# Optimization experiments

Hardware: AMD Instinct MI355X
Metric: run time of the kernel (lower is better)

## Reference

```python
import jax, jax.numpy as jnp
import numpy as np

K = 3          # kernel_size (local window)
PAD = 1        # padding = (K-1)//2 -> 'same' output size
GROUPS = 8
C_OUT = 64


def _unfold3d(x, k):
    """x: [B,C,Dp,Hp,Wp] -> [B,C,D,H,W,kd,kh,kw] sliding windows (stride 1)."""
    B, C, Dp, Hp, Wp = x.shape
    D, H, W = Dp - k + 1, Hp - k + 1, Wp - k + 1
    idx_d = jnp.arange(D)[:, None] + jnp.arange(k)[None, :]
    idx_h = jnp.arange(H)[:, None] + jnp.arange(k)[None, :]
    idx_w = jnp.arange(W)[:, None] + jnp.arange(k)[None, :]
    x = x[:, :, idx_d]              # [B,C,D,kd,Hp,Wp]
    x = x[:, :, :, :, idx_h]        # [B,C,D,kd,H,kh,Wp]
    x = x[:, :, :, :, :, :, idx_w]  # [B,C,D,kd,H,kh,W,kw]
    return jnp.transpose(x, (0, 1, 2, 4, 6, 3, 5, 7))


def setup_inputs() -> dict:
    key = jax.random.key(0)
    ks = jax.random.split(key, 7)
    B, Cin, D, H, W = 1, 64, 16, 64, 64
    c3 = C_OUT // 3                 # 21
    rest = C_OUT - 2 * c3           # 22
    fan_out_scale = np.sqrt(2.0 / C_OUT)  # kaiming_normal fan_out, relu
    x = jax.random.normal(ks[0], (B, Cin, D, H, W), dtype=jnp.float32)
    w_q = jax.random.normal(ks[1], (C_OUT, Cin), dtype=jnp.float32) * fan_out_scale
    w_k = jax.random.normal(ks[2], (C_OUT, Cin), dtype=jnp.float32) * fan_out_scale
    w_v = jax.random.normal(ks[3], (C_OUT, Cin), dtype=jnp.float32) * fan_out_scale
    rel_d = jax.random.normal(ks[4], (c3, 1, 1, 1, K, 1, 1), dtype=jnp.float32)
    rel_h = jax.random.normal(ks[5], (c3, 1, 1, 1, 1, K, 1), dtype=jnp.float32)
    rel_w = jax.random.normal(ks[6], (rest, 1, 1, 1, 1, 1, K), dtype=jnp.float32)
    return {"x": x, "w_q": w_q, "w_k": w_k, "w_v": w_v,
            "rel_d": rel_d, "rel_h": rel_h, "rel_w": rel_w}


def reference(x, w_q, w_k, w_v, rel_d, rel_h, rel_w):
    B, Cin, D, H, W = x.shape
    cg = C_OUT // GROUPS
    c3 = C_OUT // 3
    # 1x1x1 convs (bias=False): plain channel mixing. conv(pad(x)) == pad(conv(x)).
    q = jnp.einsum('oc,bcdhw->bodhw', w_q, x)
    k = jnp.einsum('oc,bcdhw->bodhw', w_k, x)
    v = jnp.einsum('oc,bcdhw->bodhw', w_v, x)
    pad = [(0, 0), (0, 0), (PAD, PAD), (PAD, PAD), (PAD, PAD)]
    k = jnp.pad(k, pad)
    v = jnp.pad(v, pad)
    k_win = _unfold3d(k, K)   # [B,Co,D,H,W,kd,kh,kw]
    v_win = _unfold3d(v, K)
    # split relative position bias across channel thirds
    k_win = jnp.concatenate([
        k_win[:, :c3] + rel_d,
        k_win[:, c3:2 * c3] + rel_h,
        k_win[:, 2 * c3:] + rel_w,
    ], axis=1)
    Kv = K * K * K
    k_win = k_win.reshape(B, GROUPS, cg, D, H, W, Kv)
    v_win = v_win.reshape(B, GROUPS, cg, D, H, W, Kv)
    qg = q.reshape(B, GROUPS, cg, D, H, W, 1)
    attn = jax.nn.softmax(qg * k_win, axis=-1)
    out = jnp.einsum('bncdhwk,bncdhwk->bncdhw', attn, v_win)
    return out.reshape(B, C_OUT, D, H, W)
```

## Files before the change

### kernel.cpp

```cpp
#include <hip/hip_runtime.h>

#define SP    65536
#define DD    16
#define HH    64
#define WW    64
#define CIN   64
#define COUT  64

#define XP    132
#define WP    68

#define LOG2E 1.44269504f


__global__ __launch_bounds__(256) void proj(const float* __restrict__ x,
                                            const float* __restrict__ wq,
                                            const float* __restrict__ wk,
                                            const float* __restrict__ wv,
                                            float* __restrict__ q,
                                            float* __restrict__ k,
                                            float* __restrict__ v) {
    __shared__ float xl[CIN][XP];
    __shared__ float wl[COUT][WP];

    const int t  = threadIdx.x;
    const int p0 = blockIdx.x * 128;
    const int m  = blockIdx.y;

    const float* __restrict__ wsel = (m == 0) ? wq : (m == 1) ? wk : wv;
    float* __restrict__       osel = (m == 0) ? q  : (m == 1) ? k  : v;

#pragma unroll
    for (int i = 0; i < 8; ++i) {
        const int f = t + 256 * i;
        const int c = f >> 5, j = f & 31;
        *(float4*)(&xl[c][j * 4]) = *(const float4*)(x + c * SP + p0 + j * 4);
    }
#pragma unroll
    for (int i = 0; i < 4; ++i) {
        const int f = t + 256 * i;
        const int o = f >> 4, j = f & 15;
        *(float4*)(&wl[o][j * 4]) = *(const float4*)(wsel + o * CIN + j * 4);
    }
    __syncthreads();

    const int og    = t >> 5;
    const int pg    = t & 31;
    const int obase = og * 8;
    const int pbase = pg * 4;

    float acc[8][4] = {};
#pragma unroll 2
    for (int c4 = 0; c4 < CIN / 4; ++c4) {
        float4 w4[8], x4[4];
#pragma unroll
        for (int i = 0; i < 8; ++i)
            w4[i] = *(const float4*)(&wl[obase + i][c4 * 4]);
#pragma unroll
        for (int cc = 0; cc < 4; ++cc)
            x4[cc] = *(const float4*)(&xl[c4 * 4 + cc][pbase]);
#pragma unroll
        for (int i = 0; i < 8; ++i) {
            const float* wf = (const float*)&w4[i];
#pragma unroll
            for (int cc = 0; cc < 4; ++cc) {
                const float* xf = (const float*)&x4[cc];
                const float wv_ = wf[cc];
                acc[i][0] = fmaf(wv_, xf[0], acc[i][0]);
                acc[i][1] = fmaf(wv_, xf[1], acc[i][1]);
                acc[i][2] = fmaf(wv_, xf[2], acc[i][2]);
                acc[i][3] = fmaf(wv_, xf[3], acc[i][3]);
            }
        }
    }

#pragma unroll
    for (int i = 0; i < 8; ++i)
        *(float4*)(osel + (obase + i) * SP + p0 + pbase) =
            make_float4(acc[i][0], acc[i][1], acc[i][2], acc[i][3]);
}

__device__ __forceinline__ float dpp_shr1(float x) {
    return __int_as_float(__builtin_amdgcn_mov_dpp(__float_as_int(x), 0x111, 0xf, 0xf, true));
}
__device__ __forceinline__ float dpp_shl1(float x) {
    return __int_as_float(__builtin_amdgcn_mov_dpp(__float_as_int(x), 0x101, 0xf, 0xf, true));
}

template<int AXIS>
__device__ __forceinline__ void attn_tile(const float* __restrict__ kt,
                                          const float* __restrict__ vt,
                                          const float (&ql)[2][4],
                                          float r0, float r1, float r2,
                                          int wg, int h, int dg,
                                          float (&s)[2][4], float (&a)[2][4]) {
#pragma unroll
    for (int nl = 0; nl < 4; ++nl) {
#pragma unroll
        for (int kh = 0; kh < 3; ++kh) {
            const int off = ((dg * 2 + nl) * 10 + h + kh) * 64 + wg * 4;
            const float4 km = *(const float4*)(kt + off);
            const float4 vm = *(const float4*)(vt + off);
            const float kl = dpp_shr1(km.w), kr = dpp_shl1(km.x);
            const float vl = dpp_shr1(vm.w), vr = dpp_shl1(vm.x);
            const float krow[6] = { kl, km.x, km.y, km.z, km.w, kr };
            const float vrow[6] = { vl, vm.x, vm.y, vm.z, vm.w, vr };

            const float rkh = (kh == 0) ? r0 : (kh == 1) ? r1 : r2;

#pragma unroll
            for (int di = 0; di < 2; ++di) {
                const int kd = nl - di;
                if (kd >= 0 && kd < 3) {
                    const float rdd = (kd == 0) ? r0 : (kd == 1) ? r1 : r2;
                    const float rr  = (AXIS == 0) ? rdd : (AXIS == 1) ? rkh : 0.f;
#pragma unroll
                    for (int wi = 0; wi < 4; ++wi) {
                        const float qv = ql[di][wi];
#pragma unroll
                        for (int kw = 0; kw < 3; ++kw) {
                            const float rc = (AXIS == 2)
                                           ? ((kw == 0) ? r0 : (kw == 1) ? r1 : r2)
                                           : rr;
                            const float e = __builtin_amdgcn_exp2f(qv * (krow[wi + kw] + rc));
                            s[di][wi] += e;
                            a[di][wi] = fmaf(e, vrow[wi + kw], a[di][wi]);
                        }
                    }
                }
            }
        }
    }
}

__global__ __launch_bounds__(256) void attn(const float* __restrict__ kbuf,
                                            const float* __restrict__ vbuf,
                                            const float* __restrict__ qbuf,
                                            const float* __restrict__ rel_d,
                                            const float* __restrict__ rel_h,
                                            const float* __restrict__ rel_w,
                                            float* __restrict__ out) {
    __shared__ float kt[60 * 64];
    __shared__ float vt[60 * 64];

    const int dt = blockIdx.x;
    const int ht = blockIdx.y;
    const int o  = blockIdx.z;

    const int d0 = dt * 4;
    const int h0 = ht * 8;
    const int t  = threadIdx.x;

    const float* __restrict__ kc = kbuf + o * SP;
    const float* __restrict__ vc = vbuf + o * SP;

#pragma unroll
    for (int i = 0; i < 8; ++i) {
        const int idx = t + 256 * i;
        if (idx < 1920) {
            const bool isv = idx >= 960;
            const int rem  = isv ? idx - 960 : idx;
            const int row  = rem >> 4;
            const int j    = rem & 15;
            const int nn   = row / 10;
            const int hp   = row - nn * 10;
            const int dpg  = d0 - 1 + nn;
            const int hpg  = h0 - 1 + hp;
            float4 val = make_float4(0.f, 0.f, 0.f, 0.f);
            if ((unsigned)dpg < (unsigned)DD && (unsigned)hpg < (unsigned)HH) {
                const float* src = (isv ? vc : kc) + (dpg * HH + hpg) * WW + j * 4;
                val = *(const float4*)src;
            }
            *(float4*)((isv ? vt : kt) + row * 64 + j * 4) = val;
        }
    }

    const int wg = t & 15;
    const int h  = (t >> 4) & 7;
    const int dg = t >> 7;

    float ql[2][4];
#pragma unroll
    for (int di = 0; di < 2; ++di) {
        const int dabs = d0 + dg * 2 + di;
        const float4 q4 = *(const float4*)(qbuf + o * SP + (dabs * HH + (h0 + h)) * WW + wg * 4);
        ql[di][0] = q4.x * LOG2E; ql[di][1] = q4.y * LOG2E;
        ql[di][2] = q4.z * LOG2E; ql[di][3] = q4.w * LOG2E;
    }

    __syncthreads();

    float s[2][4] = {};
    float a[2][4] = {};

    if (o < 21) {
        attn_tile<0>(kt, vt, ql, rel_d[o * 3 + 0], rel_d[o * 3 + 1], rel_d[o * 3 + 2],
                     wg, h, dg, s, a);
    } else if (o < 42) {
        const int b = o - 21;
        attn_tile<1>(kt, vt, ql, rel_h[b * 3 + 0], rel_h[b * 3 + 1], rel_h[b * 3 + 2],
                     wg, h, dg, s, a);
    } else {
        const int b = o - 42;
        attn_tile<2>(kt, vt, ql, rel_w[b * 3 + 0], rel_w[b * 3 + 1], rel_w[b * 3 + 2],
                     wg, h, dg, s, a);
    }

#pragma unroll
    for (int di = 0; di < 2; ++di) {
        const int dabs = d0 + dg * 2 + di;
        float4 ov;
        ov.x = a[di][0] * __builtin_amdgcn_rcpf(s[di][0]);
        ov.y = a[di][1] * __builtin_amdgcn_rcpf(s[di][1]);
        ov.z = a[di][2] * __builtin_amdgcn_rcpf(s[di][2]);
        ov.w = a[di][3] * __builtin_amdgcn_rcpf(s[di][3]);
        *(float4*)(out + o * SP + (dabs * HH + (h0 + h)) * WW + wg * 4) = ov;
    }
}

extern "C" void kernel_launch(void* const* d_in, const int* in_sizes, int n_in,
                              void* d_out, int out_size, void* d_ws, size_t ws_size,
                              hipStream_t stream) {
    const float* x     = (const float*)d_in[0];
    const float* w_q   = (const float*)d_in[1];
    const float* w_k   = (const float*)d_in[2];
    const float* w_v   = (const float*)d_in[3];
    const float* rel_d = (const float*)d_in[4];
    const float* rel_h = (const float*)d_in[5];
    const float* rel_w = (const float*)d_in[6];
    float* out = (float*)d_out;

    float* ws = (float*)d_ws;
    float* q  = ws;
    float* k  = ws + (size_t)COUT * SP;
    float* v  = ws + 2 * (size_t)COUT * SP;

    proj<<<dim3(SP / 128, 3), 256, 0, stream>>>(x, w_q, w_k, w_v, q, k, v);
    attn<<<dim3(4, 8, 64), 256, 0, stream>>>(k, v, q, rel_d, rel_h, rel_w, out);
}
```

Measured before the change: 125.7 us.

## Compute QKV projection with split-bf16 MFMA instead of FP32 FMAs

The 1x1x1 projection kernel now splits weights and inputs into hi/lo bf16 pairs in shared memory and uses 16x16x32 bf16 MFMA instructions (three products per tile: hi*hi, hi*lo, lo*hi) to approximate FP32 precision. This replaces the scalar FMA register-tiled GEMM and moves its arithmetic onto the matrix cores. In exchange it adds conversion work during staging, transposed scalar LDS stores that may bank-conflict, and uncoalesced scalar output stores. It also gives up a little accuracy relative to a true FP32 product.

```diff
diff --git a/kernel.cpp b/kernel.cpp
--- a/kernel.cpp
+++ b/kernel.cpp
@@ -7,11 +7,23 @@
 #define CIN   64
 #define COUT  64
 
-#define XP    132
-#define WP    68
-
 #define LOG2E 1.44269504f
 
+#define WPITCH 72
+#define XPITCH 72
+
+typedef short short8 __attribute__((ext_vector_type(8)));
+typedef float floatx4 __attribute__((ext_vector_type(4)));
+
+
+__device__ __forceinline__ float b2f(unsigned short u) {
+    return __uint_as_float(((unsigned)u) << 16);
+}
+__device__ __forceinline__ unsigned short f2b(float f) {
+    union { float f; unsigned u; } c; c.f = f;
+    unsigned r = c.u + 0x7fff + ((c.u >> 16) & 1);
+    return (unsigned short)(r >> 16);
+}
 
 __global__ __launch_bounds__(256) void proj(const float* __restrict__ x,
                                             const float* __restrict__ wq,
@@ -20,8 +32,10 @@
                                             float* __restrict__ q,
                                             float* __restrict__ k,
                                             float* __restrict__ v) {
-    __shared__ float xl[CIN][XP];
-    __shared__ float wl[COUT][WP];
+    __shared__ unsigned short whi[COUT * WPITCH];
+    __shared__ unsigned short wlo[COUT * WPITCH];
+    __shared__ unsigned short xhi[128 * XPITCH];
+    __shared__ unsigned short xlo[128 * XPITCH];
 
     const int t  = threadIdx.x;
     const int p0 = blockIdx.x * 128;
@@ -33,51 +47,78 @@
 #pragma unroll
     for (int i = 0; i < 8; ++i) {
         const int f = t + 256 * i;
-        const int c = f >> 5, j = f & 31;
-        *(float4*)(&xl[c][j * 4]) = *(const float4*)(x + c * SP + p0 + j * 4);
+        const int c = f >> 5;
+        const int j = f & 31;
+        const float4 val = *(const float4*)(x + c * SP + p0 + j * 4);
+        const float vf[4] = { val.x, val.y, val.z, val.w };
+#pragma unroll
+        for (int e = 0; e < 4; ++e) {
+            const int p = j * 4 + e;
+            const unsigned short h = f2b(vf[e]);
+            const float lof = vf[e] - b2f(h);
+            xhi[p * XPITCH + c] = h;
+            xlo[p * XPITCH + c] = f2b(lof);
+        }
     }
 #pragma unroll
     for (int i = 0; i < 4; ++i) {
-        const int f = t + 256 * i;
-        const int o = f >> 4, j = f & 15;
-        *(float4*)(&wl[o][j * 4]) = *(const float4*)(wsel + o * CIN + j * 4);
+        const int f  = t + 256 * i;
+        const int o  = f >> 4;
+        const int jc = f & 15;
+        const float4 val = *(const float4*)(wsel + o * CIN + jc * 4);
+        const float vf[4] = { val.x, val.y, val.z, val.w };
+        ushort4 h4, l4;
+        unsigned short* hp = (unsigned short*)&h4;
+        unsigned short* lp = (unsigned short*)&l4;
+#pragma unroll
+        for (int e = 0; e < 4; ++e) {
+            hp[e] = f2b(vf[e]);
+            lp[e] = f2b(vf[e] - b2f(hp[e]));
+        }
+        *(ushort4*)(whi + o * WPITCH + jc * 4) = h4;
+        *(ushort4*)(wlo + o * WPITCH + jc * 4) = l4;
     }
     __syncthreads();
 
-    const int og    = t >> 5;
-    const int pg    = t & 31;
-    const int obase = og * 8;
-    const int pbase = pg * 4;
-
-    float acc[8][4] = {};
-#pragma unroll 2
-    for (int c4 = 0; c4 < CIN / 4; ++c4) {
-        float4 w4[8], x4[4];
-#pragma unroll
-        for (int i = 0; i < 8; ++i)
-            w4[i] = *(const float4*)(&wl[obase + i][c4 * 4]);
-#pragma unroll
-        for (int cc = 0; cc < 4; ++cc)
-            x4[cc] = *(const float4*)(&xl[c4 * 4 + cc][pbase]);
-#pragma unroll
-        for (int i = 0; i < 8; ++i) {
-            const float* wf = (const float*)&w4[i];
-#pragma unroll
-            for (int cc = 0; cc < 4; ++cc) {
-                const float* xf = (const float*)&x4[cc];
-                const float wv_ = wf[cc];
-                acc[i][0] = fmaf(wv_, xf[0], acc[i][0]);
-                acc[i][1] = fmaf(wv_, xf[1], acc[i][1]);
-                acc[i][2] = fmaf(wv_, xf[2], acc[i][2]);
-                acc[i][3] = fmaf(wv_, xf[3], acc[i][3]);
-            }
-        }
-    }
-
-#pragma unroll
-    for (int i = 0; i < 8; ++i)
-        *(float4*)(osel + (obase + i) * SP + p0 + pbase) =
-            make_float4(acc[i][0], acc[i][1], acc[i][2], acc[i][3]);
+    const int wave  = t >> 6;
+    const int lane  = t & 63;
+    const int l15   = lane & 15;
+    const int quad  = lane >> 4;
+    const int otile = wave * 16;
+
+    short8 ahi[2], alo[2];
+#pragma unroll
+    for (int ks = 0; ks < 2; ++ks) {
+        const int off = (otile + l15) * WPITCH + ks * 32 + quad * 8;
+        ahi[ks] = *(const short8*)(whi + off);
+        alo[ks] = *(const short8*)(wlo + off);
+    }
+
+#pragma unroll
+    for (int pt = 0; pt < 8; ++pt) {
+        const int n = pt * 16 + l15;
+        short8 bhi[2], blo[2];
+#pragma unroll
+        for (int ks = 0; ks < 2; ++ks) {
+            const int off = n * XPITCH + ks * 32 + quad * 8;
+            bhi[ks] = *(const short8*)(xhi + off);
+            blo[ks] = *(const short8*)(xlo + off);
+        }
+        floatx4 acc = {0.f, 0.f, 0.f, 0.f};
+        acc = __builtin_amdgcn_mfma_f32_16x16x32_bf16(ahi[0], bhi[0], acc, 0, 0, 0);
+        acc = __builtin_amdgcn_mfma_f32_16x16x32_bf16(ahi[1], bhi[1], acc, 0, 0, 0);
+        acc = __builtin_amdgcn_mfma_f32_16x16x32_bf16(ahi[0], blo[0], acc, 0, 0, 0);
+        acc = __builtin_amdgcn_mfma_f32_16x16x32_bf16(ahi[1], blo[1], acc, 0, 0, 0);
+        acc = __builtin_amdgcn_mfma_f32_16x16x32_bf16(alo[0], bhi[0], acc, 0, 0, 0);
+        acc = __builtin_amdgcn_mfma_f32_16x16x32_bf16(alo[1], bhi[1], acc, 0, 0, 0);
+
+        const int p = p0 + pt * 16 + l15;
+#pragma unroll
+        for (int r = 0; r < 4; ++r) {
+            const int o = otile + quad * 4 + r;
+            osel[o * SP + p] = acc[r];
+        }
+    }
 }
 
 __device__ __forceinline__ float dpp_shr1(float x) {
```

New measurement: 129.2 us. 1.03x slower.
